# Kernel tuning notes

Measured on AMD Instinct MI355X. Metric: run time of the kernel, lower is better.

The kernel has to match this reference:

```python
import jax, jax.numpy as jnp
import numpy as np
import itertools

W_ASSIGN = 1.0   # options_file['assignments_loss_weight']
W_CAT = 0.5      # options_file['categorizer_loss_weight']


def _bce(p, y):
    # torch.nn.BCELoss semantics: log terms clamped at -100
    logp = jnp.clip(jnp.log(p), -100.0)
    log1mp = jnp.clip(jnp.log1p(-p), -100.0)
    return -(y * logp + (1.0 - y) * log1mp)


def setup_inputs() -> dict:
    key = jax.random.key(0)
    k0, k1, k2, k3 = jax.random.split(key, 4)
    B, P, M = 8192, 4, 12
    assignments = jax.random.uniform(k0, (B, P, M, M), dtype=jnp.float32)
    category = jax.random.uniform(k1, (B, P), dtype=jnp.float32)
    assignments_labels = jax.random.randint(k2, (B, P, M, M), 0, 2).astype(jnp.float32)
    category_labels = jax.random.randint(k3, (B, P), 0, 2).astype(jnp.float32)
    return {
        "assignments": assignments,
        "category": category,
        "assignments_labels": assignments_labels,
        "category_labels": category_labels,
    }


def reference(assignments, category, assignments_labels, category_labels):
    B, P = assignments.shape[0], assignments.shape[1]
    # All P! permutations, in itertools order (matches first-strict-min tie-break
    # of the original loop combined with argmin's first-occurrence rule).
    perms = jnp.asarray(np.array(list(itertools.permutations(range(P))), dtype=np.int32))  # [K, P]

    # [B, K, P, M, M]: assignments with slot dim permuted for every permutation
    permuted = assignments[:, perms]
    elem = _bce(permuted, assignments_labels[:, None])          # [B, K, P, M, M]
    per_perm_loss = elem.mean(axis=(2, 3, 4))                   # [B, K]

    min_loss = per_perm_loss.min(axis=1)                        # [B]
    best = jnp.argmin(per_perm_loss, axis=1)                    # [B]
    batch_perms = perms[best]                                   # [B, P]

    permuted_category = jnp.take_along_axis(category, batch_perms, axis=1)  # [B, P]

    assignments_loss = min_loss.mean()
    category_loss = _bce(permuted_category, category_labels).mean()
    return W_ASSIGN * assignments_loss + W_CAT * category_loss
```

## Files before the change

### kernel.cpp

```cpp
#include <hip/hip_runtime.h>
#include <math.h>


#define LOG2_CLIP (-144.26950408889634f)
#define LN2F      (0.6931471805599453f)

typedef int v2i __attribute__((ext_vector_type(2)));

__device__ __forceinline__ float pl32_add(float a, float b) {
    v2i r = __builtin_amdgcn_permlane32_swap(__float_as_int(a),
                                             __float_as_int(b), false, false);
    return __int_as_float(r[0]) + __int_as_float(r[1]);
}
__device__ __forceinline__ float pl16_add(float a, float b) {
    v2i r = __builtin_amdgcn_permlane16_swap(__float_as_int(a),
                                             __float_as_int(b), false, false);
    return __int_as_float(r[0]) + __int_as_float(r[1]);
}
__device__ __forceinline__ float dpp_x1(float x) {
    return __int_as_float(__builtin_amdgcn_update_dpp(
        0, __float_as_int(x), 0xB1, 0xF, 0xF, false));
}
__device__ __forceinline__ float dpp_x2(float x) {
    return __int_as_float(__builtin_amdgcn_update_dpp(
        0, __float_as_int(x), 0x4E, 0xF, 0xF, false));
}

#define PK(a,b,c,d) ((unsigned)((4u*(a)) | ((16u+4u*(b))<<8) | \
                                ((32u+4u*(c))<<16) | ((48u+4u*(d))<<24)))
__device__ const unsigned PERM_PK[32] = {
    PK(0,1,2,3), PK(0,1,3,2), PK(0,2,1,3), PK(0,2,3,1), PK(0,3,1,2), PK(0,3,2,1),
    PK(1,0,2,3), PK(1,0,3,2), PK(1,2,0,3), PK(1,2,3,0), PK(1,3,0,2), PK(1,3,2,0),
    PK(2,0,1,3), PK(2,0,3,1), PK(2,1,0,3), PK(2,1,3,0), PK(2,3,0,1), PK(2,3,1,0),
    PK(3,0,1,2), PK(3,0,2,1), PK(3,1,0,2), PK(3,1,2,0), PK(3,2,0,1), PK(3,2,1,0),
    PK(0,1,2,3), PK(0,1,2,3), PK(0,1,2,3), PK(0,1,2,3),
    PK(0,1,2,3), PK(0,1,2,3), PK(0,1,2,3), PK(0,1,2,3)
};

__global__ __launch_bounds__(256) void hsl_partial(
    const float* __restrict__ assign,
    const float* __restrict__ cat,
    const float* __restrict__ alabels,
    const float* __restrict__ clabels,
    float* __restrict__ bsums)
{
    __shared__ float lred[4];

    const int tid  = (int)threadIdx.x;
    const int wib  = tid >> 6;
    const int lane = tid & 63;
    const int b    = (int)blockIdx.x * 4 + wib;

    const float* __restrict__ A = assign  + (size_t)b * 576;
    const float* __restrict__ Y = alabels + (size_t)b * 576;

    const unsigned pk = PERM_PK[lane & 31];

    float catv;
    {
        const int gq = lane & 3;
        const int gp = (lane >> 2) & 3;
        const float cq  = cat[(size_t)b * 4 + gq];
        const float cyp = clabels[(size_t)b * 4 + gp];
        const float arg = (cyp != 0.0f) ? cq : 1.0f - cq;
        catv = fmaxf(__log2f(arg), LOG2_CLIP);
    }

    float s[16], T[4];
#pragma unroll
    for (int i = 0; i < 16; ++i) s[i] = 0.0f;
#pragma unroll
    for (int i = 0; i < 4; ++i) T[i] = 0.0f;

#pragma unroll
    for (int it = 0; it < 3; ++it) {
        if (it < 2 || lane < 16) {
            const int e = lane + it * 64;
            float d[4], y[4];
#pragma unroll
            for (int q = 0; q < 4; ++q) {
                const float a  = A[q * 144 + e];
                const float la = fmaxf(__log2f(a),        LOG2_CLIP);
                const float lb = fmaxf(__log2f(1.0f - a), LOG2_CLIP);
                d[q] = la - lb;
                T[q] += lb;
            }
#pragma unroll
            for (int p = 0; p < 4; ++p) y[p] = Y[p * 144 + e];
#pragma unroll
            for (int p = 0; p < 4; ++p)
#pragma unroll
                for (int q = 0; q < 4; ++q)
                    s[p * 4 + q] = fmaf(y[p], d[q], s[p * 4 + q]);
        }
    }
#pragma unroll
    for (int i = 0; i < 16; ++i) s[i] += T[i & 3];

    float t[8];
#pragma unroll
    for (int i = 0; i < 8; ++i) t[i] = pl32_add(s[i], s[i + 8]);
    float u[4];
#pragma unroll
    for (int i = 0; i < 4; ++i) u[i] = pl16_add(t[i], t[i + 4]);

    const bool h8 = (lane & 8) != 0;
    const bool h4 = (lane & 4) != 0;
    float w[2];
#pragma unroll
    for (int i = 0; i < 2; ++i) {
        const float keep = h8 ? u[i + 2] : u[i];
        const float send = h8 ? u[i]     : u[i + 2];
        w[i] = keep + __shfl_xor(send, 8, 64);
    }
    float x;
    {
        const float keep = h4 ? w[1] : w[0];
        const float send = h4 ? w[0] : w[1];
        x = keep + __shfl_xor(send, 4, 64);
    }
    x += dpp_x2(x);
    x += dpp_x1(x);

    const int a0 = (int)( pk        & 0xFFu);
    const int a1 = (int)((pk >> 8)  & 0xFFu);
    const int a2 = (int)((pk >> 16) & 0xFFu);
    const int a3 = (int)( pk >> 24        );
    const float v0 = __shfl(x, a0, 64);
    const float v1 = __shfl(x, a1, 64);
    const float v2 = __shfl(x, a2, 64);
    const float v3 = __shfl(x, a3, 64);
    float score = (v0 + v1) + (v2 + v3);
    if (lane >= 24) score = -__builtin_huge_valf();

    float smax = score;
    smax = fmaxf(smax, __shfl_xor(smax, 16, 64));
    smax = fmaxf(smax, __shfl_xor(smax, 8, 64));
    smax = fmaxf(smax, __shfl_xor(smax, 4, 64));
    smax = fmaxf(smax, dpp_x2(smax));
    smax = fmaxf(smax, dpp_x1(smax));

    const unsigned long long bal = __ballot(score == smax);
    const int win = (int)__builtin_ctzll(bal);
    const unsigned pkw = (unsigned)__builtin_amdgcn_readlane((int)pk, win);

    const int c0 = (int)((pkw >> 2)  & 0x0Fu);
    const int c1 = (int)((pkw >> 10) & 0x0Fu);
    const int c2 = (int)((pkw >> 18) & 0x0Fu);
    const int c3 = (int)((pkw >> 26) & 0x0Fu);
    const float g0 = __int_as_float(__builtin_amdgcn_readlane(__float_as_int(catv), c0));
    const float g1 = __int_as_float(__builtin_amdgcn_readlane(__float_as_int(catv), c1));
    const float g2 = __int_as_float(__builtin_amdgcn_readlane(__float_as_int(catv), c2));
    const float g3 = __int_as_float(__builtin_amdgcn_readlane(__float_as_int(catv), c3));
    const float csum = (g0 + g1) + (g2 + g3);

    if (lane == 0) {
        lred[wib] = -LN2F * (smax * (1.0f / 576.0f) + 0.125f * csum);
    }
    __syncthreads();

    if (tid == 0) {
        bsums[blockIdx.x] = (lred[0] + lred[1]) + (lred[2] + lred[3]);
    }
}

__global__ __launch_bounds__(256) void hsl_reduce(
    const float* __restrict__ bsums,
    float* __restrict__ out,
    int n, int B)
{
    __shared__ double sw[4];
    const int tid  = (int)threadIdx.x;
    const int wid  = tid >> 6;
    const int lane = tid & 63;

    const float4* __restrict__ v4 = (const float4*)bsums;
    const int n4 = n >> 2;
    double d = 0.0;
    for (int i = tid; i < n4; i += 256) {
        const float4 v = v4[i];
        d += (double)((v.x + v.y) + (v.z + v.w));
    }

#pragma unroll
    for (int m = 32; m >= 1; m >>= 1)
        d += __shfl_xor(d, m, 64);

    if (lane == 0) sw[wid] = d;
    __syncthreads();

    if (tid == 0) {
        const double t = (sw[0] + sw[1]) + (sw[2] + sw[3]);
        out[0] = (float)(t / (double)B);
    }
}

extern "C" void kernel_launch(void* const* d_in, const int* in_sizes, int n_in,
                              void* d_out, int out_size, void* d_ws, size_t ws_size,
                              hipStream_t stream) {
    const float* assign  = (const float*)d_in[0];
    const float* cat     = (const float*)d_in[1];
    const float* alabels = (const float*)d_in[2];
    const float* clabels = (const float*)d_in[3];
    float* out = (float*)d_out;

    const int B = in_sizes[0] / 576;
    float* bsums = (float*)d_ws;

    const int nblocks = B / 4;
    hipLaunchKernelGGL(hsl_partial, dim3(nblocks), dim3(256), 0, stream,
                       assign, cat, alabels, clabels, bsums);
    hipLaunchKernelGGL(hsl_reduce, dim3(1), dim3(256), 0, stream,
                       bsums, out, nblocks, B);
}
```

Measured before the change: 13.81 us.

## Process two batch items per wavefront with merged cross-lane reduction

Each wavefront now handles two batch samples, accumulating separate 16-entry permutation score arrays and merging them in a shared transpose-reduction tree so both samples' 4x4 costs end up in separate 32-lane halves. Permutation scoring, max, argmin and category gathers run per half-wave. The grid is halved, which amortizes the reduction and shuffle overhead per sample and gives each thread more independent loads in flight. In exchange, register pressure rises and there is less wave-level parallelism, so latency hiding across waves is reduced.

```diff
diff --git a/kernel.cpp b/kernel.cpp
--- a/kernel.cpp
+++ b/kernel.cpp
@@ -37,6 +37,37 @@
     PK(0,1,2,3), PK(0,1,2,3), PK(0,1,2,3), PK(0,1,2,3)
 };
 
+#define MAIN_LOOP(Aptr, Yptr, sacc)                                           \
+    {                                                                         \
+        float T[4];                                                           \
+        _Pragma("unroll")                                                     \
+        for (int i = 0; i < 4; ++i) T[i] = 0.0f;                              \
+        _Pragma("unroll")                                                     \
+        for (int it = 0; it < 3; ++it) {                                      \
+            if (it < 2 || lane < 16) {                                        \
+                const int e = lane + it * 64;                                 \
+                float d[4], y[4];                                             \
+                _Pragma("unroll")                                             \
+                for (int q = 0; q < 4; ++q) {                                 \
+                    const float a  = (Aptr)[q * 144 + e];                     \
+                    const float la = fmaxf(__log2f(a),        LOG2_CLIP);     \
+                    const float lb = fmaxf(__log2f(1.0f - a), LOG2_CLIP);     \
+                    d[q] = la - lb;                                           \
+                    T[q] += lb;                                               \
+                }                                                             \
+                _Pragma("unroll")                                             \
+                for (int p = 0; p < 4; ++p) y[p] = (Yptr)[p * 144 + e];       \
+                _Pragma("unroll")                                             \
+                for (int p = 0; p < 4; ++p)                                   \
+                    _Pragma("unroll")                                         \
+                    for (int q = 0; q < 4; ++q)                               \
+                        (sacc)[p * 4 + q] = fmaf(y[p], d[q], (sacc)[p * 4 + q]); \
+            }                                                                 \
+        }                                                                     \
+        _Pragma("unroll")                                                     \
+        for (int i = 0; i < 16; ++i) (sacc)[i] += T[i & 3];                   \
+    }
+
 __global__ __launch_bounds__(256) void hsl_partial(
     const float* __restrict__ assign,
     const float* __restrict__ cat,
@@ -49,89 +80,73 @@
     const int tid  = (int)threadIdx.x;
     const int wib  = tid >> 6;
     const int lane = tid & 63;
-    const int b    = (int)blockIdx.x * 4 + wib;
-
-    const float* __restrict__ A = assign  + (size_t)b * 576;
-    const float* __restrict__ Y = alabels + (size_t)b * 576;
+    const int base = ((int)blockIdx.x * 4 + wib) * 2;
+
+    const float* __restrict__ A0 = assign  + (size_t)base * 576;
+    const float* __restrict__ Y0 = alabels + (size_t)base * 576;
+    const float* __restrict__ A1 = A0 + 576;
+    const float* __restrict__ Y1 = Y0 + 576;
 
     const unsigned pk = PERM_PK[lane & 31];
 
     float catv;
     {
-        const int gq = lane & 3;
-        const int gp = (lane >> 2) & 3;
-        const float cq  = cat[(size_t)b * 4 + gq];
-        const float cyp = clabels[(size_t)b * 4 + gp];
+        const int bb  = base + (lane >> 5);
+        const float cq  = cat[(size_t)bb * 4 + (lane & 3)];
+        const float cyp = clabels[(size_t)bb * 4 + ((lane >> 2) & 3)];
         const float arg = (cyp != 0.0f) ? cq : 1.0f - cq;
         catv = fmaxf(__log2f(arg), LOG2_CLIP);
     }
 
-    float s[16], T[4];
-#pragma unroll
-    for (int i = 0; i < 16; ++i) s[i] = 0.0f;
-#pragma unroll
-    for (int i = 0; i < 4; ++i) T[i] = 0.0f;
-
-#pragma unroll
-    for (int it = 0; it < 3; ++it) {
-        if (it < 2 || lane < 16) {
-            const int e = lane + it * 64;
-            float d[4], y[4];
-#pragma unroll
-            for (int q = 0; q < 4; ++q) {
-                const float a  = A[q * 144 + e];
-                const float la = fmaxf(__log2f(a),        LOG2_CLIP);
-                const float lb = fmaxf(__log2f(1.0f - a), LOG2_CLIP);
-                d[q] = la - lb;
-                T[q] += lb;
-            }
-#pragma unroll
-            for (int p = 0; p < 4; ++p) y[p] = Y[p * 144 + e];
-#pragma unroll
-            for (int p = 0; p < 4; ++p)
-#pragma unroll
-                for (int q = 0; q < 4; ++q)
-                    s[p * 4 + q] = fmaf(y[p], d[q], s[p * 4 + q]);
-        }
-    }
-#pragma unroll
-    for (int i = 0; i < 16; ++i) s[i] += T[i & 3];
-
-    float t[8];
-#pragma unroll
-    for (int i = 0; i < 8; ++i) t[i] = pl32_add(s[i], s[i + 8]);
-    float u[4];
-#pragma unroll
-    for (int i = 0; i < 4; ++i) u[i] = pl16_add(t[i], t[i + 4]);
+    float s0[16], s1[16];
+#pragma unroll
+    for (int i = 0; i < 16; ++i) { s0[i] = 0.0f; s1[i] = 0.0f; }
+    MAIN_LOOP(A0, Y0, s0)
+    MAIN_LOOP(A1, Y1, s1)
+
+    float m[16];
+#pragma unroll
+    for (int i = 0; i < 16; ++i) m[i] = pl32_add(s0[i], s1[i]);
+    float u[8];
+#pragma unroll
+    for (int i = 0; i < 8; ++i) u[i] = pl16_add(m[i], m[i + 8]);
 
     const bool h8 = (lane & 8) != 0;
     const bool h4 = (lane & 4) != 0;
-    float w[2];
+    const bool h2 = (lane & 2) != 0;
+    float w[4];
+#pragma unroll
+    for (int i = 0; i < 4; ++i) {
+        const float keep = h8 ? u[i + 4] : u[i];
+        const float send = h8 ? u[i]     : u[i + 4];
+        w[i] = keep + __shfl_xor(send, 8, 64);
+    }
+    float v[2];
 #pragma unroll
     for (int i = 0; i < 2; ++i) {
-        const float keep = h8 ? u[i + 2] : u[i];
-        const float send = h8 ? u[i]     : u[i + 2];
-        w[i] = keep + __shfl_xor(send, 8, 64);
+        const float keep = h4 ? w[i + 2] : w[i];
+        const float send = h4 ? w[i]     : w[i + 2];
+        v[i] = keep + __shfl_xor(send, 4, 64);
     }
     float x;
     {
-        const float keep = h4 ? w[1] : w[0];
-        const float send = h4 ? w[0] : w[1];
-        x = keep + __shfl_xor(send, 4, 64);
-    }
-    x += dpp_x2(x);
+        const float keep = h2 ? v[1] : v[0];
+        const float send = h2 ? v[0] : v[1];
+        x = keep + __shfl_xor(send, 2, 64);
+    }
     x += dpp_x1(x);
 
-    const int a0 = (int)( pk        & 0xFFu);
-    const int a1 = (int)((pk >> 8)  & 0xFFu);
-    const int a2 = (int)((pk >> 16) & 0xFFu);
-    const int a3 = (int)( pk >> 24        );
+    const int hb = (int)(lane & 32);
+    const int a0 = (int)((pk >>  1) & 0x7Fu) | hb;
+    const int a1 = (int)((pk >>  9) & 0x7Fu) | hb;
+    const int a2 = (int)((pk >> 17) & 0x7Fu) | hb;
+    const int a3 = (int)((pk >> 25) & 0x7Fu) | hb;
     const float v0 = __shfl(x, a0, 64);
     const float v1 = __shfl(x, a1, 64);
     const float v2 = __shfl(x, a2, 64);
     const float v3 = __shfl(x, a3, 64);
     float score = (v0 + v1) + (v2 + v3);
-    if (lane >= 24) score = -__builtin_huge_valf();
+    if ((lane & 31) >= 24) score = -__builtin_huge_valf();
 
     float smax = score;
     smax = fmaxf(smax, __shfl_xor(smax, 16, 64));
@@ -141,21 +156,24 @@
     smax = fmaxf(smax, dpp_x1(smax));
 
     const unsigned long long bal = __ballot(score == smax);
-    const int win = (int)__builtin_ctzll(bal);
-    const unsigned pkw = (unsigned)__builtin_amdgcn_readlane((int)pk, win);
-
-    const int c0 = (int)((pkw >> 2)  & 0x0Fu);
-    const int c1 = (int)((pkw >> 10) & 0x0Fu);
-    const int c2 = (int)((pkw >> 18) & 0x0Fu);
-    const int c3 = (int)((pkw >> 26) & 0x0Fu);
-    const float g0 = __int_as_float(__builtin_amdgcn_readlane(__float_as_int(catv), c0));
-    const float g1 = __int_as_float(__builtin_amdgcn_readlane(__float_as_int(catv), c1));
-    const float g2 = __int_as_float(__builtin_amdgcn_readlane(__float_as_int(catv), c2));
-    const float g3 = __int_as_float(__builtin_amdgcn_readlane(__float_as_int(catv), c3));
-    const float csum = (g0 + g1) + (g2 + g3);
+    const int win0 = (int)__builtin_ctzll(bal & 0xFFFFFFFFULL);
+    const int win1 = 32 + (int)__builtin_ctzll(bal >> 32);
+    const unsigned pkw0 = (unsigned)__builtin_amdgcn_readlane((int)pk, win0);
+    const unsigned pkw1 = (unsigned)__builtin_amdgcn_readlane((int)pk, win1);
+    const float sm0 = __int_as_float(__builtin_amdgcn_readlane(__float_as_int(smax), 0));
+    const float sm1 = __int_as_float(__builtin_amdgcn_readlane(__float_as_int(smax), 32));
+
+#define CATR(pkw, off, sh) __int_as_float(__builtin_amdgcn_readlane( \
+        __float_as_int(catv), (int)(((pkw) >> (sh)) & 0x0Fu) + (off)))
+    const float csum0 = (CATR(pkw0, 0, 2)  + CATR(pkw0, 0, 10))
+                      + (CATR(pkw0, 0, 18) + CATR(pkw0, 0, 26));
+    const float csum1 = (CATR(pkw1, 32, 2)  + CATR(pkw1, 32, 10))
+                      + (CATR(pkw1, 32, 18) + CATR(pkw1, 32, 26));
+#undef CATR
 
     if (lane == 0) {
-        lred[wib] = -LN2F * (smax * (1.0f / 576.0f) + 0.125f * csum);
+        lred[wib] = -LN2F * ((sm0 + sm1) * (1.0f / 576.0f)
+                             + 0.125f * (csum0 + csum1));
     }
     __syncthreads();
 
@@ -183,8 +201,8 @@
     }
 
 #pragma unroll
-    for (int m = 32; m >= 1; m >>= 1)
-        d += __shfl_xor(d, m, 64);
+    for (int m2 = 32; m2 >= 1; m2 >>= 1)
+        d += __shfl_xor(d, m2, 64);
 
     if (lane == 0) sw[wid] = d;
     __syncthreads();
@@ -207,7 +225,7 @@
     const int B = in_sizes[0] / 576;
     float* bsums = (float*)d_ws;
 
-    const int nblocks = B / 4;
+    const int nblocks = B / 8;
     hipLaunchKernelGGL(hsl_partial, dim3(nblocks), dim3(256), 0, stream,
                        assign, cat, alabels, clabels, bsums);
     hipLaunchKernelGGL(hsl_reduce, dim3(1), dim3(256), 0, stream,
```

Measured after the change: 13.91 us. About the same (+0.7%).
